# Kernel tuning notes

Measured on AMD Instinct MI355X. Metric: run time of the kernel, lower is better.

Reference implementation:

```python
import jax, jax.numpy as jnp
import numpy as np


def gcn_conv(x, edge_index, W, b):
    # PyG GCNConv: h = x @ W; add self-loops; symmetric D^-1/2 (A+I) D^-1/2 aggregation; + bias
    n = x.shape[0]
    h = x @ W  # [N, out]
    loop = jnp.arange(n, dtype=edge_index.dtype)
    src = jnp.concatenate([edge_index[0], loop])  # message sources
    dst = jnp.concatenate([edge_index[1], loop])  # message targets
    ones = jnp.ones(dst.shape[0], dtype=h.dtype)
    deg = jax.ops.segment_sum(ones, dst, num_segments=n)  # in-degree incl. self-loop
    dinv = jnp.where(deg > 0, jax.lax.rsqrt(deg), 0.0)
    norm = dinv[src] * dinv[dst]  # [E+N]
    msg = h[src] * norm[:, None]  # gather + scale
    out = jax.ops.segment_sum(msg, dst, num_segments=n)  # scatter-add
    return out + b


def setup_inputs() -> dict:
    key = jax.random.key(0)
    ks = jax.random.split(key, 6)
    N, E, D = 100000, 600000, 128
    x = jax.random.normal(ks[0], (N, D), dtype=jnp.float32)
    edge_index = jax.random.randint(ks[1], (2, E), 0, N, dtype=jnp.int64)
    s = 1.0 / np.sqrt(D)
    W1 = jax.random.normal(ks[2], (D, D), dtype=jnp.float32) * s
    b1 = jnp.zeros((D,), dtype=jnp.float32)
    W2 = jax.random.normal(ks[3], (2 * D, D), dtype=jnp.float32) * (1.0 / np.sqrt(2 * D))
    b2 = jnp.zeros((D,), dtype=jnp.float32)
    Wout = jax.random.normal(ks[4], (D, 1), dtype=jnp.float32) * s
    bout = jnp.zeros((1,), dtype=jnp.float32)
    return {"x": x, "edge_index": edge_index, "W1": W1, "b1": b1,
            "W2": W2, "b2": b2, "Wout": Wout, "bout": bout}


def reference(x, edge_index, W1, b1, W2, b2, Wout, bout):
    y = gcn_conv(x, edge_index, W1, b1)          # [N, D]
    y = jnp.concatenate([x, y], axis=-1)          # [N, 2D]
    y = jax.nn.leaky_relu(y, negative_slope=0.01)
    z = gcn_conv(y, edge_index, W2, b2)           # [N, D]
    z = jax.nn.leaky_relu(z, negative_slope=0.01)
    return z @ Wout + bout                        # [N, 1]
```

## Files before the change

kernel.cpp:

```cpp
#include <hip/hip_runtime.h>

#define DIM 128
#define CAP 48

typedef _Float16 half8 __attribute__((ext_vector_type(8)));
typedef float f32x4 __attribute__((ext_vector_type(4)));

__device__ __forceinline__ float lrelu(float v) { return v > 0.f ? v : 0.01f * v; }

__global__ __launch_bounds__(256) void k_prep(
    const int* __restrict__ src, const int* __restrict__ dst,
    int* __restrict__ cursor, int* __restrict__ srcs, int e, int eb,
    const float* __restrict__ W1, _Float16* __restrict__ Wp1,
    const float* __restrict__ W2, _Float16* __restrict__ Wp2) {
    int b = blockIdx.x;
    if (b < eb) {
        int i = b * 256 + threadIdx.x;
        if (i < e) {
            int d = dst[i];
            int p = atomicAdd(&cursor[d], 1);
            if (p < CAP) srcs[(size_t)d * CAP + p] = src[i];
        }
        return;
    }
    b -= eb;
    const float* W;
    _Float16* Wp;
    int tid2;
    if (b < 64) { W = W1; Wp = Wp1; tid2 = b * 256 + threadIdx.x; }
    else        { W = W2; Wp = Wp2; tid2 = (b - 64) * 256 + threadIdx.x; }
    int jj = tid2 & 7;
    int frag = tid2 >> 3;
    int l = frag & 63;
    int cb = (frag >> 6) & 7;
    int kb = frag >> 9;
    int k = kb * 32 + ((l >> 4) << 3) + jj;
    int nn = cb * 16 + (l & 15);
    Wp[tid2] = (_Float16)W[(size_t)k * DIM + nn];
}

__global__ __launch_bounds__(256, 2) void k_mm1(
    const float* __restrict__ x, const _Float16* __restrict__ Wp1,
    const _Float16* __restrict__ Wp2, const int* __restrict__ cursor,
    _Float16* __restrict__ hs, _Float16* __restrict__ P, int n) {
    const int tid = threadIdx.x;
    const int w = tid >> 6, l = tid & 63;
    const int row0 = blockIdx.x * 64;
    const int arow = row0 + w * 16 + (l & 15);
    const int kq = (l >> 4) << 3;
    const bool ok = arow < n;
    const float* xr = &x[(size_t)arow * DIM + kq];

    f32x4 ah[8], ap[8];
#pragma unroll
    for (int cb = 0; cb < 8; ++cb) {
        f32x4 z = {0.f, 0.f, 0.f, 0.f};
        ah[cb] = z; ap[cb] = z;
    }

#pragma unroll
    for (int kb = 0; kb < 4; ++kb) {
        float4 v0 = make_float4(0.f, 0.f, 0.f, 0.f), v1 = v0;
        if (ok) {
            v0 = *(const float4*)&xr[kb * 32];
            v1 = *(const float4*)&xr[kb * 32 + 4];
        }
        half8 a, al;
        a[0] = (_Float16)v0.x; a[1] = (_Float16)v0.y;
        a[2] = (_Float16)v0.z; a[3] = (_Float16)v0.w;
        a[4] = (_Float16)v1.x; a[5] = (_Float16)v1.y;
        a[6] = (_Float16)v1.z; a[7] = (_Float16)v1.w;
#pragma unroll
        for (int e = 0; e < 8; ++e) {
            _Float16 t = a[e];
            al[e] = (t > (_Float16)0.f) ? t : t * (_Float16)0.01f;
        }
#pragma unroll
        for (int cb = 0; cb < 8; ++cb) {
            half8 bf = *(const half8*)&Wp1[((kb * 8 + cb) * 64 + l) * 8];
            ah[cb] = __builtin_amdgcn_mfma_f32_16x16x32_f16(a, bf, ah[cb], 0, 0, 0);
        }
#pragma unroll
        for (int cb = 0; cb < 8; ++cb) {
            half8 bf = *(const half8*)&Wp2[((kb * 8 + cb) * 64 + l) * 8];
            ap[cb] = __builtin_amdgcn_mfma_f32_16x16x32_f16(al, bf, ap[cb], 0, 0, 0);
        }
    }
    const int orow0 = row0 + w * 16 + ((l >> 4) << 2);
    const int oc = l & 15;
#pragma unroll
    for (int reg = 0; reg < 4; ++reg) {
        int grow = orow0 + reg;
        if (grow < n) {
            float d = rsqrtf((float)cursor[grow] + 1.0f);
#pragma unroll
            for (int cb = 0; cb < 8; ++cb)
                hs[(size_t)grow * DIM + cb * 16 + oc] = (_Float16)(ah[cb][reg] * d);
        }
    }
    _Float16* pl = P + ((size_t)(blockIdx.x * 4 + w) * 64 + l) * 32;
#pragma unroll
    for (int c = 0; c < 4; ++c) {
        half8 o;
#pragma unroll
        for (int e = 0; e < 4; ++e) {
            o[e]     = (_Float16)ap[2 * c][e];
            o[4 + e] = (_Float16)ap[2 * c + 1][e];
        }
        *(half8*)&pl[c * 8] = o;
    }
}

__global__ __launch_bounds__(256, 2) void k_mm2g(
    const _Float16* __restrict__ hs, const int* __restrict__ cursor,
    const int* __restrict__ srcs, const float* __restrict__ b1,
    const _Float16* __restrict__ Wp2, const _Float16* __restrict__ P,
    _Float16* __restrict__ hs2, int n) {
    __shared__ _Float16 Af[16 * 64 * 8];
    const int tid = threadIdx.x;
    const int w = tid >> 6, l = tid & 63;
    const int row0 = blockIdx.x * 64;

    f32x4 acc[8];
    const _Float16* pl = P + ((size_t)(blockIdx.x * 4 + w) * 64 + l) * 32;
#pragma unroll
    for (int c = 0; c < 4; ++c) {
        half8 pv = *(const half8*)&pl[c * 8];
#pragma unroll
        for (int e = 0; e < 4; ++e) {
            acc[2 * c][e]     = (float)pv[e];
            acc[2 * c + 1][e] = (float)pv[4 + e];
        }
    }

    const int g = tid & 15;
#pragma unroll
    for (int it = 0; it < 4; ++it) {
        int node = row0 + it * 16 + (tid >> 4);
        half8 o = 0;
        if (node < n) {
            int rawc = cursor[node];
            float d = rsqrtf((float)rawc + 1.0f);
            int cnt = rawc > CAP ? CAP : rawc;
            const int* sl = &srcs[(size_t)node * CAP];
            half8 h = *(const half8*)&hs[(size_t)node * DIM + g * 8];
            float a[8];
#pragma unroll
            for (int e = 0; e < 8; ++e) a[e] = (float)h[e];
            for (int base = 0; base < cnt; base += 16) {
                int m = cnt - base;
                if (m > 16) m = 16;
                int sid = (g < m) ? sl[base + g] : 0;
#pragma unroll 4
                for (int j = 0; j < m; ++j) {
                    int s = __shfl(sid, j, 16);
                    half8 v = *(const half8*)&hs[(size_t)s * DIM + g * 8];
#pragma unroll
                    for (int e = 0; e < 8; ++e) a[e] += (float)v[e];
                }
            }
            const float4 bb0 = *(const float4*)&b1[g * 8];
            const float4 bb1 = *(const float4*)&b1[g * 8 + 4];
            o[0] = (_Float16)lrelu(fmaf(a[0], d, bb0.x));
            o[1] = (_Float16)lrelu(fmaf(a[1], d, bb0.y));
            o[2] = (_Float16)lrelu(fmaf(a[2], d, bb0.z));
            o[3] = (_Float16)lrelu(fmaf(a[3], d, bb0.w));
            o[4] = (_Float16)lrelu(fmaf(a[4], d, bb1.x));
            o[5] = (_Float16)lrelu(fmaf(a[5], d, bb1.y));
            o[6] = (_Float16)lrelu(fmaf(a[6], d, bb1.z));
            o[7] = (_Float16)lrelu(fmaf(a[7], d, bb1.w));
        }
        *(half8*)&Af[(((it * 4 + (g >> 2)) * 64) + (g & 3) * 16 + (tid >> 4)) * 8] = o;
    }
    __syncthreads();

#pragma unroll
    for (int kb = 0; kb < 4; ++kb) {
        half8 a = *(const half8*)&Af[((w * 4 + kb) * 64 + l) * 8];
#pragma unroll
        for (int cb = 0; cb < 8; ++cb) {
            half8 bf = *(const half8*)&Wp2[(((kb + 4) * 8 + cb) * 64 + l) * 8];
            acc[cb] = __builtin_amdgcn_mfma_f32_16x16x32_f16(a, bf, acc[cb], 0, 0, 0);
        }
    }
    const int orow0 = row0 + w * 16 + ((l >> 4) << 2);
    const int oc = l & 15;
#pragma unroll
    for (int reg = 0; reg < 4; ++reg) {
        int grow = orow0 + reg;
        if (grow < n) {
            float d = rsqrtf((float)cursor[grow] + 1.0f);
#pragma unroll
            for (int cb = 0; cb < 8; ++cb)
                hs2[(size_t)grow * DIM + cb * 16 + oc] = (_Float16)(acc[cb][reg] * d);
        }
    }
}

__global__ __launch_bounds__(256) void k_gather2(
    const _Float16* __restrict__ hs2, const int* __restrict__ cursor,
    const int* __restrict__ srcs, const float* __restrict__ b2,
    const float* __restrict__ wout, const float* __restrict__ bout,
    float* __restrict__ out, int n) {
    const int node = blockIdx.x * 16 + (threadIdx.x >> 4);
    const int g = threadIdx.x & 15;
    if (node >= n) return;
    int rawc = cursor[node];
    float d = rsqrtf((float)rawc + 1.0f);
    int cnt = rawc > CAP ? CAP : rawc;
    const int* sl = &srcs[(size_t)node * CAP];
    half8 h = *(const half8*)&hs2[(size_t)node * DIM + g * 8];
    float a[8];
#pragma unroll
    for (int e = 0; e < 8; ++e) a[e] = (float)h[e];
    for (int base = 0; base < cnt; base += 16) {
        int m = cnt - base;
        if (m > 16) m = 16;
        int sid = (g < m) ? sl[base + g] : 0;
#pragma unroll 4
        for (int j = 0; j < m; ++j) {
            int s = __shfl(sid, j, 16);
            half8 v = *(const half8*)&hs2[(size_t)s * DIM + g * 8];
#pragma unroll
            for (int e = 0; e < 8; ++e) a[e] += (float)v[e];
        }
    }
    const float4 bb0 = *(const float4*)&b2[g * 8];
    const float4 bb1 = *(const float4*)&b2[g * 8 + 4];
    const float4 wv0 = *(const float4*)&wout[g * 8];
    const float4 wv1 = *(const float4*)&wout[g * 8 + 4];
    float s = lrelu(fmaf(a[0], d, bb0.x)) * wv0.x + lrelu(fmaf(a[1], d, bb0.y)) * wv0.y +
              lrelu(fmaf(a[2], d, bb0.z)) * wv0.z + lrelu(fmaf(a[3], d, bb0.w)) * wv0.w +
              lrelu(fmaf(a[4], d, bb1.x)) * wv1.x + lrelu(fmaf(a[5], d, bb1.y)) * wv1.y +
              lrelu(fmaf(a[6], d, bb1.z)) * wv1.z + lrelu(fmaf(a[7], d, bb1.w)) * wv1.w;
#pragma unroll
    for (int off = 8; off > 0; off >>= 1) s += __shfl_down(s, off, 16);
    if (g == 0) out[node] = s + bout[0];
}

extern "C" void kernel_launch(void* const* d_in, const int* in_sizes, int n_in,
                              void* d_out, int out_size, void* d_ws, size_t ws_size,
                              hipStream_t stream) {
    const float* x    = (const float*)d_in[0];
    const int*   ei   = (const int*)d_in[1];
    const float* W1   = (const float*)d_in[2];
    const float* b1   = (const float*)d_in[3];
    const float* W2   = (const float*)d_in[4];
    const float* b2   = (const float*)d_in[5];
    const float* Wout = (const float*)d_in[6];
    const float* bout = (const float*)d_in[7];
    float* out = (float*)d_out;

    const int N = in_sizes[0] / DIM;
    const int E = in_sizes[1] / 2;
    const int* src = ei;
    const int* dst = ei + E;

    const int gb = (N + 63) / 64;

    size_t Na = ((size_t)N + 63) & ~(size_t)63;
    int* cursor   = (int*)d_ws;
    int* srcs     = cursor + Na;
    _Float16* Wp1 = (_Float16*)(srcs + (size_t)N * CAP);
    _Float16* Wp2 = Wp1 + 128 * 128;
    _Float16* hsb = Wp2 + 256 * 128;
    _Float16* Pb  = hsb + (size_t)N * DIM;

    const int eb = (E + 255) / 256;
    const int ab = (N + 15) / 16;

    hipMemsetAsync(cursor, 0, (size_t)N * sizeof(int), stream);
    k_prep<<<eb + 64 + 128, 256, 0, stream>>>(src, dst, cursor, srcs, E, eb, W1, Wp1, W2, Wp2);
    k_mm1<<<gb, 256, 0, stream>>>(x, Wp1, Wp2, cursor, hsb, Pb, N);
    k_mm2g<<<gb, 256, 0, stream>>>(hsb, cursor, srcs, b1, Wp2, Pb, Pb, N);
    k_gather2<<<ab, 256, 0, stream>>>(Pb, cursor, srcs, b2, Wout, bout, out, N);
}
```

Measured before the change: 234.3 us.

## Pre-convert x to fp16, stage outputs via LDS, use wave-wide neighbor gather

Converts x to fp16 inside the prep kernel so mm1 reads half-width inputs. Stages the mm1 and mm2g output tiles through padded shared memory so global stores are coalesced 16-byte rows. Restructures both gather kernels to use a full wavefront per node, with four neighbors processed in parallel and then reduced via cross-lane shuffles. This trades an extra conversion pass and fewer concurrent nodes per block for coalescing and more memory parallelism per node.

After: 270.7 us. 1.16x slower.

```diff
diff --git a/kernel.cpp b/kernel.cpp
--- a/kernel.cpp
+++ b/kernel.cpp
@@ -12,7 +12,8 @@
     const int* __restrict__ src, const int* __restrict__ dst,
     int* __restrict__ cursor, int* __restrict__ srcs, int e, int eb,
     const float* __restrict__ W1, _Float16* __restrict__ Wp1,
-    const float* __restrict__ W2, _Float16* __restrict__ Wp2) {
+    const float* __restrict__ W2, _Float16* __restrict__ Wp2,
+    const float* __restrict__ x, _Float16* __restrict__ xh, long long nx) {
     int b = blockIdx.x;
     if (b < eb) {
         int i = b * 256 + threadIdx.x;
@@ -24,32 +25,48 @@
         return;
     }
     b -= eb;
-    const float* W;
-    _Float16* Wp;
-    int tid2;
-    if (b < 64) { W = W1; Wp = Wp1; tid2 = b * 256 + threadIdx.x; }
-    else        { W = W2; Wp = Wp2; tid2 = (b - 64) * 256 + threadIdx.x; }
-    int jj = tid2 & 7;
-    int frag = tid2 >> 3;
-    int l = frag & 63;
-    int cb = (frag >> 6) & 7;
-    int kb = frag >> 9;
-    int k = kb * 32 + ((l >> 4) << 3) + jj;
-    int nn = cb * 16 + (l & 15);
-    Wp[tid2] = (_Float16)W[(size_t)k * DIM + nn];
+    if (b < 192) {
+        const float* W;
+        _Float16* Wp;
+        int tid2;
+        if (b < 64) { W = W1; Wp = Wp1; tid2 = b * 256 + threadIdx.x; }
+        else        { W = W2; Wp = Wp2; tid2 = (b - 64) * 256 + threadIdx.x; }
+        int jj = tid2 & 7;
+        int frag = tid2 >> 3;
+        int l = frag & 63;
+        int cb = (frag >> 6) & 7;
+        int kb = frag >> 9;
+        int k = kb * 32 + ((l >> 4) << 3) + jj;
+        int nn = cb * 16 + (l & 15);
+        Wp[tid2] = (_Float16)W[(size_t)k * DIM + nn];
+        return;
+    }
+    b -= 192;
+    long long i0 = ((long long)b * 256 + threadIdx.x) * 8;
+    if (i0 < nx) {
+        float4 v0 = *(const float4*)&x[i0];
+        float4 v1 = *(const float4*)&x[i0 + 4];
+        half8 o;
+        o[0] = (_Float16)v0.x; o[1] = (_Float16)v0.y;
+        o[2] = (_Float16)v0.z; o[3] = (_Float16)v0.w;
+        o[4] = (_Float16)v1.x; o[5] = (_Float16)v1.y;
+        o[6] = (_Float16)v1.z; o[7] = (_Float16)v1.w;
+        *(half8*)&xh[i0] = o;
+    }
 }
 
 __global__ __launch_bounds__(256, 2) void k_mm1(
-    const float* __restrict__ x, const _Float16* __restrict__ Wp1,
+    const _Float16* __restrict__ xh, const _Float16* __restrict__ Wp1,
     const _Float16* __restrict__ Wp2, const int* __restrict__ cursor,
     _Float16* __restrict__ hs, _Float16* __restrict__ P, int n) {
+    __shared__ _Float16 Hs[64 * 136];
     const int tid = threadIdx.x;
     const int w = tid >> 6, l = tid & 63;
     const int row0 = blockIdx.x * 64;
     const int arow = row0 + w * 16 + (l & 15);
     const int kq = (l >> 4) << 3;
     const bool ok = arow < n;
-    const float* xr = &x[(size_t)arow * DIM + kq];
+    const _Float16* xr = &xh[(size_t)arow * DIM + kq];
 
     f32x4 ah[8], ap[8];
 #pragma unroll
@@ -60,16 +77,9 @@
 
 #pragma unroll
     for (int kb = 0; kb < 4; ++kb) {
-        float4 v0 = make_float4(0.f, 0.f, 0.f, 0.f), v1 = v0;
-        if (ok) {
-            v0 = *(const float4*)&xr[kb * 32];
-            v1 = *(const float4*)&xr[kb * 32 + 4];
-        }
-        half8 a, al;
-        a[0] = (_Float16)v0.x; a[1] = (_Float16)v0.y;
-        a[2] = (_Float16)v0.z; a[3] = (_Float16)v0.w;
-        a[4] = (_Float16)v1.x; a[5] = (_Float16)v1.y;
-        a[6] = (_Float16)v1.z; a[7] = (_Float16)v1.w;
+        half8 a = 0;
+        if (ok) a = *(const half8*)&xr[kb * 32];
+        half8 al;
 #pragma unroll
         for (int e = 0; e < 8; ++e) {
             _Float16 t = a[e];
@@ -86,17 +96,23 @@
             ap[cb] = __builtin_amdgcn_mfma_f32_16x16x32_f16(al, bf, ap[cb], 0, 0, 0);
         }
     }
-    const int orow0 = row0 + w * 16 + ((l >> 4) << 2);
+    const int orow = w * 16 + ((l >> 4) << 2);
     const int oc = l & 15;
 #pragma unroll
     for (int reg = 0; reg < 4; ++reg) {
-        int grow = orow0 + reg;
-        if (grow < n) {
-            float d = rsqrtf((float)cursor[grow] + 1.0f);
-#pragma unroll
-            for (int cb = 0; cb < 8; ++cb)
-                hs[(size_t)grow * DIM + cb * 16 + oc] = (_Float16)(ah[cb][reg] * d);
-        }
+        int grow = row0 + orow + reg;
+        float d = (grow < n) ? rsqrtf((float)cursor[grow] + 1.0f) : 0.f;
+#pragma unroll
+        for (int cb = 0; cb < 8; ++cb)
+            Hs[(orow + reg) * 136 + cb * 16 + oc] = (_Float16)(ah[cb][reg] * d);
+    }
+    __syncthreads();
+#pragma unroll
+    for (int it = 0; it < 4; ++it) {
+        int i = it * 256 + tid;
+        int r = i >> 4, c = (i & 15) * 8;
+        if (row0 + r < n)
+            *(half8*)&hs[(size_t)(row0 + r) * DIM + c] = *(const half8*)&Hs[r * 136 + c];
     }
     _Float16* pl = P + ((size_t)(blockIdx.x * 4 + w) * 64 + l) * 32;
 #pragma unroll
@@ -116,9 +132,10 @@
     const int* __restrict__ srcs, const float* __restrict__ b1,
     const _Float16* __restrict__ Wp2, const _Float16* __restrict__ P,
     _Float16* __restrict__ hs2, int n) {
-    __shared__ _Float16 Af[16 * 64 * 8];
+    __shared__ _Float16 LS[64 * 136];
     const int tid = threadIdx.x;
     const int w = tid >> 6, l = tid & 63;
+    const int g = l & 15, eq = l >> 4;
     const int row0 = blockIdx.x * 64;
 
     f32x4 acc[8];
@@ -133,67 +150,75 @@
         }
     }
 
-    const int g = tid & 15;
-#pragma unroll
-    for (int it = 0; it < 4; ++it) {
-        int node = row0 + it * 16 + (tid >> 4);
-        half8 o = 0;
+    for (int s = 0; s < 16; ++s) {
+        int node = row0 + w * 16 + s;
         if (node < n) {
             int rawc = cursor[node];
-            float d = rsqrtf((float)rawc + 1.0f);
             int cnt = rawc > CAP ? CAP : rawc;
-            const int* sl = &srcs[(size_t)node * CAP];
+            int sidall = (l < cnt) ? srcs[(size_t)node * CAP + l] : 0;
             half8 h = *(const half8*)&hs[(size_t)node * DIM + g * 8];
             float a[8];
 #pragma unroll
-            for (int e = 0; e < 8; ++e) a[e] = (float)h[e];
-            for (int base = 0; base < cnt; base += 16) {
-                int m = cnt - base;
-                if (m > 16) m = 16;
-                int sid = (g < m) ? sl[base + g] : 0;
-#pragma unroll 4
-                for (int j = 0; j < m; ++j) {
-                    int s = __shfl(sid, j, 16);
-                    half8 v = *(const half8*)&hs[(size_t)s * DIM + g * 8];
+            for (int e = 0; e < 8; ++e) a[e] = (eq == 0) ? (float)h[e] : 0.f;
+            int iters = (cnt + 3) >> 2;
+            for (int t = 0; t < iters; ++t) {
+                int idx = t * 4 + eq;
+                int sj = __shfl(sidall, idx, 64);
+                if (idx < cnt) {
+                    half8 v = *(const half8*)&hs[(size_t)sj * DIM + g * 8];
 #pragma unroll
                     for (int e = 0; e < 8; ++e) a[e] += (float)v[e];
                 }
             }
-            const float4 bb0 = *(const float4*)&b1[g * 8];
-            const float4 bb1 = *(const float4*)&b1[g * 8 + 4];
-            o[0] = (_Float16)lrelu(fmaf(a[0], d, bb0.x));
-            o[1] = (_Float16)lrelu(fmaf(a[1], d, bb0.y));
-            o[2] = (_Float16)lrelu(fmaf(a[2], d, bb0.z));
-            o[3] = (_Float16)lrelu(fmaf(a[3], d, bb0.w));
-            o[4] = (_Float16)lrelu(fmaf(a[4], d, bb1.x));
-            o[5] = (_Float16)lrelu(fmaf(a[5], d, bb1.y));
-            o[6] = (_Float16)lrelu(fmaf(a[6], d, bb1.z));
-            o[7] = (_Float16)lrelu(fmaf(a[7], d, bb1.w));
-        }
-        *(half8*)&Af[(((it * 4 + (g >> 2)) * 64) + (g & 3) * 16 + (tid >> 4)) * 8] = o;
-    }
-    __syncthreads();
-
+#pragma unroll
+            for (int e = 0; e < 8; ++e) {
+                a[e] += __shfl_xor(a[e], 16, 64);
+                a[e] += __shfl_xor(a[e], 32, 64);
+            }
+            if (eq == 0) {
+                float d = rsqrtf((float)rawc + 1.0f);
+                const float4 bb0 = *(const float4*)&b1[g * 8];
+                const float4 bb1 = *(const float4*)&b1[g * 8 + 4];
+                half8 o;
+                o[0] = (_Float16)lrelu(fmaf(a[0], d, bb0.x));
+                o[1] = (_Float16)lrelu(fmaf(a[1], d, bb0.y));
+                o[2] = (_Float16)lrelu(fmaf(a[2], d, bb0.z));
+                o[3] = (_Float16)lrelu(fmaf(a[3], d, bb0.w));
+                o[4] = (_Float16)lrelu(fmaf(a[4], d, bb1.x));
+                o[5] = (_Float16)lrelu(fmaf(a[5], d, bb1.y));
+                o[6] = (_Float16)lrelu(fmaf(a[6], d, bb1.z));
+                o[7] = (_Float16)lrelu(fmaf(a[7], d, bb1.w));
+                *(half8*)&LS[(((w * 4 + (g >> 2)) * 64) + (g & 3) * 16 + s) * 8] = o;
+            }
+        }
+    }
 #pragma unroll
     for (int kb = 0; kb < 4; ++kb) {
-        half8 a = *(const half8*)&Af[((w * 4 + kb) * 64 + l) * 8];
+        half8 a = *(const half8*)&LS[((w * 4 + kb) * 64 + l) * 8];
 #pragma unroll
         for (int cb = 0; cb < 8; ++cb) {
             half8 bf = *(const half8*)&Wp2[(((kb + 4) * 8 + cb) * 64 + l) * 8];
             acc[cb] = __builtin_amdgcn_mfma_f32_16x16x32_f16(a, bf, acc[cb], 0, 0, 0);
         }
     }
-    const int orow0 = row0 + w * 16 + ((l >> 4) << 2);
+    __syncthreads();
+    const int orow = w * 16 + ((l >> 4) << 2);
     const int oc = l & 15;
 #pragma unroll
     for (int reg = 0; reg < 4; ++reg) {
-        int grow = orow0 + reg;
-        if (grow < n) {
-            float d = rsqrtf((float)cursor[grow] + 1.0f);
-#pragma unroll
-            for (int cb = 0; cb < 8; ++cb)
-                hs2[(size_t)grow * DIM + cb * 16 + oc] = (_Float16)(acc[cb][reg] * d);
-        }
+        int grow = row0 + orow + reg;
+        float d = (grow < n) ? rsqrtf((float)cursor[grow] + 1.0f) : 0.f;
+#pragma unroll
+        for (int cb = 0; cb < 8; ++cb)
+            LS[(orow + reg) * 136 + cb * 16 + oc] = (_Float16)(acc[cb][reg] * d);
+    }
+    __syncthreads();
+#pragma unroll
+    for (int it = 0; it < 4; ++it) {
+        int i = it * 256 + tid;
+        int r = i >> 4, c = (i & 15) * 8;
+        if (row0 + r < n)
+            *(half8*)&hs2[(size_t)(row0 + r) * DIM + c] = *(const half8*)&LS[r * 136 + c];
     }
 }
 
@@ -202,40 +227,46 @@
     const int* __restrict__ srcs, const float* __restrict__ b2,
     const float* __restrict__ wout, const float* __restrict__ bout,
     float* __restrict__ out, int n) {
-    const int node = blockIdx.x * 16 + (threadIdx.x >> 4);
-    const int g = threadIdx.x & 15;
+    const int w = threadIdx.x >> 6, l = threadIdx.x & 63;
+    const int g = l & 15, eq = l >> 4;
+    const int node = blockIdx.x * 4 + w;
     if (node >= n) return;
     int rawc = cursor[node];
-    float d = rsqrtf((float)rawc + 1.0f);
     int cnt = rawc > CAP ? CAP : rawc;
-    const int* sl = &srcs[(size_t)node * CAP];
+    int sidall = (l < cnt) ? srcs[(size_t)node * CAP + l] : 0;
     half8 h = *(const half8*)&hs2[(size_t)node * DIM + g * 8];
     float a[8];
 #pragma unroll
-    for (int e = 0; e < 8; ++e) a[e] = (float)h[e];
-    for (int base = 0; base < cnt; base += 16) {
-        int m = cnt - base;
-        if (m > 16) m = 16;
-        int sid = (g < m) ? sl[base + g] : 0;
-#pragma unroll 4
-        for (int j = 0; j < m; ++j) {
-            int s = __shfl(sid, j, 16);
-            half8 v = *(const half8*)&hs2[(size_t)s * DIM + g * 8];
+    for (int e = 0; e < 8; ++e) a[e] = (eq == 0) ? (float)h[e] : 0.f;
+    int iters = (cnt + 3) >> 2;
+    for (int t = 0; t < iters; ++t) {
+        int idx = t * 4 + eq;
+        int sj = __shfl(sidall, idx, 64);
+        if (idx < cnt) {
+            half8 v = *(const half8*)&hs2[(size_t)sj * DIM + g * 8];
 #pragma unroll
             for (int e = 0; e < 8; ++e) a[e] += (float)v[e];
         }
     }
-    const float4 bb0 = *(const float4*)&b2[g * 8];
-    const float4 bb1 = *(const float4*)&b2[g * 8 + 4];
-    const float4 wv0 = *(const float4*)&wout[g * 8];
-    const float4 wv1 = *(const float4*)&wout[g * 8 + 4];
-    float s = lrelu(fmaf(a[0], d, bb0.x)) * wv0.x + lrelu(fmaf(a[1], d, bb0.y)) * wv0.y +
-              lrelu(fmaf(a[2], d, bb0.z)) * wv0.z + lrelu(fmaf(a[3], d, bb0.w)) * wv0.w +
-              lrelu(fmaf(a[4], d, bb1.x)) * wv1.x + lrelu(fmaf(a[5], d, bb1.y)) * wv1.y +
-              lrelu(fmaf(a[6], d, bb1.z)) * wv1.z + lrelu(fmaf(a[7], d, bb1.w)) * wv1.w;
-#pragma unroll
-    for (int off = 8; off > 0; off >>= 1) s += __shfl_down(s, off, 16);
-    if (g == 0) out[node] = s + bout[0];
+#pragma unroll
+    for (int e = 0; e < 8; ++e) {
+        a[e] += __shfl_xor(a[e], 16, 64);
+        a[e] += __shfl_xor(a[e], 32, 64);
+    }
+    if (eq == 0) {
+        float d = rsqrtf((float)rawc + 1.0f);
+        const float4 bb0 = *(const float4*)&b2[g * 8];
+        const float4 bb1 = *(const float4*)&b2[g * 8 + 4];
+        const float4 wv0 = *(const float4*)&wout[g * 8];
+        const float4 wv1 = *(const float4*)&wout[g * 8 + 4];
+        float s = lrelu(fmaf(a[0], d, bb0.x)) * wv0.x + lrelu(fmaf(a[1], d, bb0.y)) * wv0.y +
+                  lrelu(fmaf(a[2], d, bb0.z)) * wv0.z + lrelu(fmaf(a[3], d, bb0.w)) * wv0.w +
+                  lrelu(fmaf(a[4], d, bb1.x)) * wv1.x + lrelu(fmaf(a[5], d, bb1.y)) * wv1.y +
+                  lrelu(fmaf(a[6], d, bb1.z)) * wv1.z + lrelu(fmaf(a[7], d, bb1.w)) * wv1.w;
+#pragma unroll
+        for (int off = 8; off > 0; off >>= 1) s += __shfl_down(s, off, 16);
+        if (g == 0) out[node] = s + bout[0];
+    }
 }
 
 extern "C" void kernel_launch(void* const* d_in, const int* in_sizes, int n_in,
@@ -257,21 +288,24 @@
     const int* dst = ei + E;
 
     const int gb = (N + 63) / 64;
+    const long long nx = (long long)N * DIM;
 
     size_t Na = ((size_t)N + 63) & ~(size_t)63;
     int* cursor   = (int*)d_ws;
     int* srcs     = cursor + Na;
     _Float16* Wp1 = (_Float16*)(srcs + (size_t)N * CAP);
     _Float16* Wp2 = Wp1 + 128 * 128;
-    _Float16* hsb = Wp2 + 256 * 128;
-    _Float16* Pb  = hsb + (size_t)N * DIM;
+    _Float16* xhb = Wp2 + 256 * 128;
+    _Float16* hsb = xhb + nx;
+    _Float16* Pb  = hsb + nx;
 
     const int eb = (E + 255) / 256;
-    const int ab = (N + 15) / 16;
+    const int cvb = (int)((nx + 2047) / 2048);
 
     hipMemsetAsync(cursor, 0, (size_t)N * sizeof(int), stream);
-    k_prep<<<eb + 64 + 128, 256, 0, stream>>>(src, dst, cursor, srcs, E, eb, W1, Wp1, W2, Wp2);
-    k_mm1<<<gb, 256, 0, stream>>>(x, Wp1, Wp2, cursor, hsb, Pb, N);
+    k_prep<<<eb + 192 + cvb, 256, 0, stream>>>(src, dst, cursor, srcs, E, eb,
+                                               W1, Wp1, W2, Wp2, x, xhb, nx);
+    k_mm1<<<gb, 256, 0, stream>>>(xhb, Wp1, Wp2, cursor, hsb, Pb, N);
     k_mm2g<<<gb, 256, 0, stream>>>(hsb, cursor, srcs, b1, Wp2, Pb, Pb, N);
-    k_gather2<<<ab, 256, 0, stream>>>(Pb, cursor, srcs, b2, Wout, bout, out, N);
-}
+    k_gather2<<<(N + 3) / 4, 256, 0, stream>>>(Pb, cursor, srcs, b2, Wout, bout, out, N);
+}
```
